# Optimization experiments

Measured on AMD Instinct MI355X. Metric: run time of the kernel, lower is better.

## Reference

```python
import jax, jax.numpy as jnp
import numpy as np


def setup_inputs() -> dict:
    key = jax.random.key(0)
    ks = jax.random.split(key, 7)
    B, S, C, H, W = 4, 8, 256, 64, 64
    A = 256
    return {
        "x": jax.random.normal(ks[0], (B, S, C, H, W), dtype=jnp.float32),
        "wq": jax.random.normal(ks[1], (A, C), dtype=jnp.float32) * (1.0 / np.sqrt(C)),
        "bq": jax.random.normal(ks[2], (A,), dtype=jnp.float32) * 0.01,
        "wk": jax.random.normal(ks[3], (A, C), dtype=jnp.float32) * (1.0 / np.sqrt(C)),
        "bk": jax.random.normal(ks[4], (A,), dtype=jnp.float32) * 0.01,
        "wv": jax.random.normal(ks[5], (A, C), dtype=jnp.float32) * (1.0 / np.sqrt(C)),
        "bv": jax.random.normal(ks[6], (A,), dtype=jnp.float32) * 0.01,
    }


def reference(x, wq, bq, wk, bk, wv, bv):
    B, S, C, H, W = x.shape
    A = wq.shape[0]
    HW = H * W
    scale = 1.0 / (A ** 0.5)

    # 1x1 conv == channel GEMM over flattened spatial dims: [B*S, C, HW] -> [B*S, A, HW]
    xr = x.reshape(B * S, C, HW)
    q = jnp.einsum('ncp,ac->nap', xr, wq) + bq[None, :, None]
    k = jnp.einsum('ncp,ac->nap', xr, wk) + bk[None, :, None]
    v = jnp.einsum('ncp,ac->nap', xr, wv) + bv[None, :, None]

    # [B, S, A, HW]
    q = q.reshape(B, S, A, HW)
    k = k.reshape(B, S, A, HW)
    v = v.reshape(B, S, A, HW)

    # Faithful to torch permute+contiguous().view: raw row-major reinterpretation
    # of the trailing [A, S] block as [S, A] (not a transpose).
    q = jnp.transpose(q, (0, 3, 2, 1)).reshape(B * HW, S, A)
    k = jnp.transpose(k, (0, 3, 1, 2)).reshape(B * HW, A, S)
    v = jnp.transpose(v, (0, 3, 2, 1)).reshape(B * HW, S, A)

    scores = jnp.einsum('nsa,nat->nst', q, k) * scale  # [B*HW, S, S]
    weights = jax.nn.softmax(scores, axis=-1)
    attended = jnp.einsum('nst,nta->nsa', weights, v)  # [B*HW, S, A]

    # view(B, H, W, A, S) raw reshape, then permute(0,4,3,1,2) -> [B, S, A, H, W]
    attended = attended.reshape(B, H, W, A, S)
    attended = jnp.transpose(attended, (0, 4, 3, 1, 2)).reshape(B, S, A, H, W)
    return attended
```

## Files before the change

### kernel.cpp

```cpp
#include <hip/hip_runtime.h>
#include <hip/hip_bf16.h>

typedef __hip_bfloat16 bf16;
typedef __attribute__((ext_vector_type(8))) short short8;
typedef __attribute__((ext_vector_type(4))) float f32x4;

#define MFMA16(A, B, C) __builtin_amdgcn_mfma_f32_16x16x32_bf16((A), (B), (C), 0, 0, 0)

__device__ __forceinline__ void bar_lds() {
    asm volatile("s_waitcnt lgkmcnt(0)\n\ts_barrier" ::: "memory");
}

__device__ __forceinline__ unsigned pkbf(float a, float b) {
    __hip_bfloat162 h2 = __float22bfloat162_rn(make_float2(a, b));
    return *reinterpret_cast<unsigned*>(&h2);
}

__global__ __launch_bounds__(256) void prep_w(const float* __restrict__ wq,
                                              const float* __restrict__ wk,
                                              const float* __restrict__ wv,
                                              bf16* __restrict__ wsW)
{
    const int t = (int)blockIdx.x * 256 + (int)threadIdx.x;
    const int lane = t & 63, kk = (t >> 6) & 7, mt = (t >> 9) & 15, proj = t >> 13;
    const float* W = (proj == 0) ? wq : ((proj == 1) ? wk : wv);
    const int row = mt * 16 + (lane & 15);
    const int col = kk * 32 + (lane >> 4) * 8;
    bf16* dst = wsW + (size_t)t * 8;
#pragma unroll
    for (int j = 0; j < 8; ++j) dst[j] = __float2bfloat16(W[row * 256 + col + j]);
}

#define QLB 8192
#define KLB 41984
#define VLB 8192
#define PLB 75776

__global__ __launch_bounds__(512, 4)
void fused_sa(const float* __restrict__ x,
              const float* __restrict__ bq, const float* __restrict__ bk,
              const float* __restrict__ bv,
              const bf16* __restrict__ wsW,
              float* __restrict__ out)
{
    __shared__ __align__(16) char SM[76928];

    const int tid = (int)threadIdx.x;
    const int l = tid & 63, w = tid >> 6, h = l >> 4, c15 = l & 15;
    const int p = c15 & 7, beta = c15 >> 3;

    const int wg = ((int)blockIdx.x & 7) * 256 + ((int)blockIdx.x >> 3);
    const int b = wg >> 9, p0 = (wg & 511) * 8;

    const short8* wsv = (const short8*)wsW;
    const int p2 = (l & 3) * 2, chi = l >> 2;
    const size_t xbase = ((size_t)((b * 8 + w) * 256)) * 4096 + p0 + p2;

    f32x4 aQ0[4] = {}, aQ1[4] = {}, aK0[4] = {}, aK1[4] = {};
    {
        float2 xr[4];
#pragma unroll
        for (int i = 0; i < 4; ++i)
            xr[i] = *(const float2*)&x[xbase + (size_t)(i * 16 + chi) * 4096];

        for (int cc = 0; cc < 4; ++cc) {
            if (cc) bar_lds();
#pragma unroll
            for (int i = 0; i < 4; ++i) {
                const int c = i * 16 + chi;
                const int r0 = w * 8 + p2, r1 = r0 + 1;
                *(bf16*)(SM + ((r0 * 128 + c * 2) ^ ((r0 & 7) << 4))) = __float2bfloat16(xr[i].x);
                *(bf16*)(SM + ((r1 * 128 + c * 2) ^ ((r1 & 7) << 4))) = __float2bfloat16(xr[i].y);
            }
            if (cc < 3) {
#pragma unroll
                for (int i = 0; i < 4; ++i)
                    xr[i] = *(const float2*)&x[xbase + (size_t)((cc + 1) * 64 + i * 16 + chi) * 4096];
            }
            bar_lds();
#pragma unroll
            for (int k2 = 0; k2 < 2; ++k2) {
                const int kg = cc * 2 + k2;
                const short8 fQ0 = wsv[((0 * 16 + 2 * w)     * 8 + kg) * 64 + l];
                const short8 fQ1 = wsv[((0 * 16 + 2 * w + 1) * 8 + kg) * 64 + l];
                const short8 fK0 = wsv[((1 * 16 + 2 * w)     * 8 + kg) * 64 + l];
                const short8 fK1 = wsv[((1 * 16 + 2 * w + 1) * 8 + kg) * 64 + l];
#pragma unroll
                for (int nt = 0; nt < 4; ++nt) {
                    const int row = nt * 16 + c15;
                    const short8 bx = *(const short8*)(SM +
                        ((row * 128 + (k2 * 32 + h * 8) * 2) ^ ((row & 7) << 4)));
                    aQ0[nt] = MFMA16(fQ0, bx, aQ0[nt]);
                    aQ1[nt] = MFMA16(fQ1, bx, aQ1[nt]);
                    aK0[nt] = MFMA16(fK0, bx, aK0[nt]);
                    aK1[nt] = MFMA16(fK1, bx, aK1[nt]);
                }
            }
        }
    }

    {
        const float4 b0 = *(const float4*)&bq[(2 * w) * 16 + 4 * h];
        const float4 b1 = *(const float4*)&bq[(2 * w + 1) * 16 + 4 * h];
        const float b0v[4] = {b0.x, b0.y, b0.z, b0.w}, b1v[4] = {b1.x, b1.y, b1.z, b1.w};
#pragma unroll
        for (int r = 0; r < 4; ++r) {
            unsigned wds[4];
#pragma unroll
            for (int nt = 0; nt < 4; ++nt) {
                const float a0 = aQ0[nt][r] + b0v[r];
                const float a1 = aQ1[nt][r] + b1v[r];
                const float send = beta ? a0 : a1;
                const float recv = __shfl_xor(send, 8);
                const float own  = beta ? a1 : a0;
                wds[nt] = beta ? pkbf(recv, own) : pkbf(own, recv);
            }
            const int G = 16 * beta + 4 * h + r;
            *(uint4*)(SM + QLB + ((p * 4224 + w * 528 + G * 16) ^ ((p & 7) << 4))) =
                make_uint4(wds[0], wds[1], wds[2], wds[3]);
        }
    }
    {
        const float4 b0 = *(const float4*)&bk[(2 * w) * 16 + 4 * h];
        const float4 b1 = *(const float4*)&bk[(2 * w + 1) * 16 + 4 * h];
        const float b0v[4] = {b0.x, b0.y, b0.z, b0.w}, b1v[4] = {b1.x, b1.y, b1.z, b1.w};
        const bool lower = (h < 2);
#pragma unroll
        for (int r = 0; r < 4; ++r) {
            const int t = 4 * (h & 1) + r;
#pragma unroll
            for (int nt = 0; nt < 4; ++nt) {
                const float a0 = aK0[nt][r] + b0v[r];
                const float a1 = aK1[nt][r] + b1v[r];
                const float r0 = __shfl_xor(a0, 32);
                const float r1 = __shfl_xor(a1, 32);
                const float j0 = lower ? a0 : r0;
                const float j1 = lower ? r0 : a0;
                const float j2 = lower ? a1 : r1;
                const float j3 = lower ? r1 : a1;
                if ((nt & 1) == (h >> 1)) {
                    const int a = ((2 * nt + beta) * 4 + (w >> 1)) * 8 + (w & 1) * 4;
                    *(uint2*)(SM + KLB + ((p * 4224 + t * 528 + a * 2) ^ ((p & 7) << 4))) =
                        make_uint2(pkbf(j0, j1), pkbf(j2, j3));
                }
            }
        }
    }
    bar_lds();

    if (w < 4) {
        const int q = w, pxr = c15 >> 3, st = c15 & 7;
        const int px = 2 * q + pxr;
        f32x4 sacc = {0.f, 0.f, 0.f, 0.f};
#pragma unroll
        for (int kk = 0; kk < 8; ++kk) {
            const int off = (px * 4224 + st * 528 + (kk * 32 + h * 8) * 2) ^ ((px & 7) << 4);
            const short8 qa = *(const short8*)(SM + QLB + off);
            const short8 kb = *(const short8*)(SM + KLB + off);
            sacc = MFMA16(qa, kb, sacc);
        }
        const bool valid = ((h >> 1) == pxr);
        const int pxo = 2 * q + (h >> 1);
        bf16 (*PL)[9][8] = (bf16 (*)[9][8])(SM + PLB);
#pragma unroll
        for (int r = 0; r < 4; ++r) {
            const float S = sacc[r] * 0.0625f;
            float m = S;
            m = fmaxf(m, __shfl_xor(m, 1));
            m = fmaxf(m, __shfl_xor(m, 2));
            m = fmaxf(m, __shfl_xor(m, 4));
            const float e = __expf(S - m);
            float sm = e;
            sm += __shfl_xor(sm, 1);
            sm += __shfl_xor(sm, 2);
            sm += __shfl_xor(sm, 4);
            if (valid) PL[pxo][4 * (h & 1) + r][st] = __float2bfloat16(e / sm);
        }
    }
    bar_lds();

    const int Mv = ((w >> 1) << 2) | (w & 1);
    f32x4 aV0[4] = {}, aV1[4] = {};
    {
        float2 xr[4];
#pragma unroll
        for (int i = 0; i < 4; ++i)
            xr[i] = *(const float2*)&x[xbase + (size_t)(i * 16 + chi) * 4096];

        for (int cc = 0; cc < 4; ++cc) {
            bar_lds();
#pragma unroll
            for (int i = 0; i < 4; ++i) {
                const int c = i * 16 + chi;
                const int r0 = w * 8 + p2, r1 = r0 + 1;
                *(bf16*)(SM + ((r0 * 128 + c * 2) ^ ((r0 & 7) << 4))) = __float2bfloat16(xr[i].x);
                *(bf16*)(SM + ((r1 * 128 + c * 2) ^ ((r1 & 7) << 4))) = __float2bfloat16(xr[i].y);
            }
            if (cc < 3) {
#pragma unroll
                for (int i = 0; i < 4; ++i)
                    xr[i] = *(const float2*)&x[xbase + (size_t)((cc + 1) * 64 + i * 16 + chi) * 4096];
            }
            bar_lds();
#pragma unroll
            for (int k2 = 0; k2 < 2; ++k2) {
                const int kg = cc * 2 + k2;
                const short8 fV0 = wsv[((2 * 16 + Mv)     * 8 + kg) * 64 + l];
                const short8 fV1 = wsv[((2 * 16 + Mv + 2) * 8 + kg) * 64 + l];
#pragma unroll
                for (int nt = 0; nt < 4; ++nt) {
                    const int row = nt * 16 + c15;
                    const short8 bx = *(const short8*)(SM +
                        ((row * 128 + (k2 * 32 + h * 8) * 2) ^ ((row & 7) << 4)));
                    aV0[nt] = MFMA16(fV0, bx, aV0[nt]);
                    aV1[nt] = MFMA16(fV1, bx, aV1[nt]);
                }
            }
        }
    }

    {
        const float4 b0 = *(const float4*)&bv[Mv * 16 + 4 * h];
        const float4 b1 = *(const float4*)&bv[(Mv + 2) * 16 + 4 * h];
        const float b0v[4] = {b0.x, b0.y, b0.z, b0.w}, b1v[4] = {b1.x, b1.y, b1.z, b1.w};
        const int tp2 = 2 * (w >> 1);
#pragma unroll
        for (int r = 0; r < 4; ++r)
#pragma unroll
            for (int nt = 0; nt < 4; ++nt) {
                const unsigned wd = pkbf(aV0[nt][r] + b0v[r], aV1[nt][r] + b1v[r]);
                const int aV = (16 * (w & 1) + 4 * h + r) * 8 + 2 * nt + beta;
                *(unsigned*)(SM + VLB +
                    ((p * 4096 + aV * 16 + tp2 * 2) ^ (((p ^ (aV >> 3)) & 7) << 4))) = wd;
            }
    }
    bar_lds();

    {
        bf16 (*PL)[9][8] = (bf16 (*)[9][8])(SM + PLB);
        const int pxl = c15 & 3, sl = c15 >> 2;
        const short8 zv = {0, 0, 0, 0, 0, 0, 0, 0};
#pragma unroll
        for (int sg = 0; sg < 2; ++sg) {
            short8 pa[2];
#pragma unroll
            for (int q = 0; q < 2; ++q) {
                const short8 t8 = *(const short8*)&PL[q * 4 + pxl][sg * 4 + sl][0];
                pa[q] = (h == pxl) ? t8 : zv;
            }
            const int s = sg * 4 + h;
#pragma unroll
            for (int ci = 0; ci < 2; ++ci) {
                const int a = (2 * w + ci) * 16 + c15;
                const int s2 = a & 7, a2 = (s << 5) | (a >> 3);
#pragma unroll
                for (int q = 0; q < 2; ++q) {
                    const int px = q * 4 + h;
                    const short8 vb = *(const short8*)(SM + VLB +
                        ((px * 4096 + a * 16) ^ (((px ^ (a >> 3)) & 7) << 4)));
                    f32x4 pacc = {0.f, 0.f, 0.f, 0.f};
                    pacc = MFMA16(pa[q], vb, pacc);
                    *(f32x4*)&out[((size_t)((b * 8 + s2) * 256 + a2)) * 4096 + p0 + q * 4] = pacc;
                }
            }
        }
    }
}

extern "C" void kernel_launch(void* const* d_in, const int* in_sizes, int n_in,
                              void* d_out, int out_size, void* d_ws, size_t ws_size,
                              hipStream_t stream) {
    (void)in_sizes; (void)n_in; (void)out_size; (void)ws_size;
    const float* x  = (const float*)d_in[0];
    const float* wq = (const float*)d_in[1];
    const float* bq = (const float*)d_in[2];
    const float* wk = (const float*)d_in[3];
    const float* bk = (const float*)d_in[4];
    const float* wv = (const float*)d_in[5];
    const float* bv = (const float*)d_in[6];
    float* out = (float*)d_out;
    bf16* wsW  = (bf16*)d_ws;

    hipLaunchKernelGGL(prep_w, dim3(96), dim3(256), 0, stream, wq, wk, wv, wsW);
    hipLaunchKernelGGL(fused_sa, dim3(2048), dim3(512), 0, stream,
                       x, bq, bk, bv, wsW, out);
}
```

Before: 172.5 us.

## Process 16 pixels per block in two halves to write 64-byte output runs

Each block now covers 16 spatial positions instead of 8 and runs the Q/K/softmax and V/PV phases twice, once per 8-pixel half. Probabilities for both halves stay in an enlarged LDS buffer, and the first half's PV results are held in registers. Once the second half is done, each output row is written as 64 contiguous bytes rather than 32-byte pieces. The aim is better write coalescing and half as many blocks, at the cost of more registers, more LDS and less parallelism.

```diff
diff --git a/kernel.cpp b/kernel.cpp
--- a/kernel.cpp
+++ b/kernel.cpp
@@ -36,6 +36,91 @@
 #define VLB 8192
 #define PLB 75776
 
+__device__ __forceinline__ void stage_chunk(char* SM, const float2* xr, int w, int p2, int chi) {
+#pragma unroll
+    for (int i = 0; i < 4; ++i) {
+        const int c = i * 16 + chi;
+        const int r0 = w * 8 + p2, r1 = r0 + 1;
+        *(bf16*)(SM + ((r0 * 128 + c * 2) ^ ((r0 & 7) << 4))) = __float2bfloat16(xr[i].x);
+        *(bf16*)(SM + ((r1 * 128 + c * 2) ^ ((r1 & 7) << 4))) = __float2bfloat16(xr[i].y);
+    }
+}
+
+__device__ __forceinline__ void qk_pass(char* SM, const short8* wsv, const float* x,
+                                        size_t xbase, int l, int w, int h, int c15,
+                                        f32x4 (&aQ0)[4], f32x4 (&aQ1)[4],
+                                        f32x4 (&aK0)[4], f32x4 (&aK1)[4])
+{
+    const int p2 = (l & 3) * 2, chi = l >> 2;
+    float2 xr[4];
+#pragma unroll
+    for (int i = 0; i < 4; ++i)
+        xr[i] = *(const float2*)&x[xbase + (size_t)(i * 16 + chi) * 4096];
+    for (int cc = 0; cc < 4; ++cc) {
+        bar_lds();
+        stage_chunk(SM, xr, w, p2, chi);
+        if (cc < 3) {
+#pragma unroll
+            for (int i = 0; i < 4; ++i)
+                xr[i] = *(const float2*)&x[xbase + (size_t)((cc + 1) * 64 + i * 16 + chi) * 4096];
+        }
+        bar_lds();
+#pragma unroll
+        for (int k2 = 0; k2 < 2; ++k2) {
+            const int kg = cc * 2 + k2;
+            const short8 fQ0 = wsv[((0 * 16 + 2 * w)     * 8 + kg) * 64 + l];
+            const short8 fQ1 = wsv[((0 * 16 + 2 * w + 1) * 8 + kg) * 64 + l];
+            const short8 fK0 = wsv[((1 * 16 + 2 * w)     * 8 + kg) * 64 + l];
+            const short8 fK1 = wsv[((1 * 16 + 2 * w + 1) * 8 + kg) * 64 + l];
+#pragma unroll
+            for (int nt = 0; nt < 4; ++nt) {
+                const int row = nt * 16 + c15;
+                const short8 bx = *(const short8*)(SM +
+                    ((row * 128 + (k2 * 32 + h * 8) * 2) ^ ((row & 7) << 4)));
+                aQ0[nt] = MFMA16(fQ0, bx, aQ0[nt]);
+                aQ1[nt] = MFMA16(fQ1, bx, aQ1[nt]);
+                aK0[nt] = MFMA16(fK0, bx, aK0[nt]);
+                aK1[nt] = MFMA16(fK1, bx, aK1[nt]);
+            }
+        }
+    }
+}
+
+__device__ __forceinline__ void v_pass(char* SM, const short8* wsv, const float* x,
+                                       size_t xbase, int l, int w, int h, int c15, int Mv,
+                                       f32x4 (&aV0)[4], f32x4 (&aV1)[4])
+{
+    const int p2 = (l & 3) * 2, chi = l >> 2;
+    float2 xr[4];
+#pragma unroll
+    for (int i = 0; i < 4; ++i)
+        xr[i] = *(const float2*)&x[xbase + (size_t)(i * 16 + chi) * 4096];
+    for (int cc = 0; cc < 4; ++cc) {
+        bar_lds();
+        stage_chunk(SM, xr, w, p2, chi);
+        if (cc < 3) {
+#pragma unroll
+            for (int i = 0; i < 4; ++i)
+                xr[i] = *(const float2*)&x[xbase + (size_t)((cc + 1) * 64 + i * 16 + chi) * 4096];
+        }
+        bar_lds();
+#pragma unroll
+        for (int k2 = 0; k2 < 2; ++k2) {
+            const int kg = cc * 2 + k2;
+            const short8 fV0 = wsv[((2 * 16 + Mv)     * 8 + kg) * 64 + l];
+            const short8 fV1 = wsv[((2 * 16 + Mv + 2) * 8 + kg) * 64 + l];
+#pragma unroll
+            for (int nt = 0; nt < 4; ++nt) {
+                const int row = nt * 16 + c15;
+                const short8 bx = *(const short8*)(SM +
+                    ((row * 128 + (k2 * 32 + h * 8) * 2) ^ ((row & 7) << 4)));
+                aV0[nt] = MFMA16(fV0, bx, aV0[nt]);
+                aV1[nt] = MFMA16(fV1, bx, aV1[nt]);
+            }
+        }
+    }
+}
+
 __global__ __launch_bounds__(512, 4)
 void fused_sa(const float* __restrict__ x,
               const float* __restrict__ bq, const float* __restrict__ bk,
@@ -43,224 +128,185 @@
               const bf16* __restrict__ wsW,
               float* __restrict__ out)
 {
-    __shared__ __align__(16) char SM[76928];
+    __shared__ __align__(16) char SM[78080];
 
     const int tid = (int)threadIdx.x;
     const int l = tid & 63, w = tid >> 6, h = l >> 4, c15 = l & 15;
     const int p = c15 & 7, beta = c15 >> 3;
 
-    const int wg = ((int)blockIdx.x & 7) * 256 + ((int)blockIdx.x >> 3);
-    const int b = wg >> 9, p0 = (wg & 511) * 8;
+    const int wg = ((int)blockIdx.x & 7) * 128 + ((int)blockIdx.x >> 3);
+    const int b = wg >> 8, p0 = (wg & 255) * 16;
 
     const short8* wsv = (const short8*)wsW;
-    const int p2 = (l & 3) * 2, chi = l >> 2;
-    const size_t xbase = ((size_t)((b * 8 + w) * 256)) * 4096 + p0 + p2;
-
-    f32x4 aQ0[4] = {}, aQ1[4] = {}, aK0[4] = {}, aK1[4] = {};
-    {
-        float2 xr[4];
-#pragma unroll
-        for (int i = 0; i < 4; ++i)
-            xr[i] = *(const float2*)&x[xbase + (size_t)(i * 16 + chi) * 4096];
-
-        for (int cc = 0; cc < 4; ++cc) {
-            if (cc) bar_lds();
-#pragma unroll
-            for (int i = 0; i < 4; ++i) {
-                const int c = i * 16 + chi;
-                const int r0 = w * 8 + p2, r1 = r0 + 1;
-                *(bf16*)(SM + ((r0 * 128 + c * 2) ^ ((r0 & 7) << 4))) = __float2bfloat16(xr[i].x);
-                *(bf16*)(SM + ((r1 * 128 + c * 2) ^ ((r1 & 7) << 4))) = __float2bfloat16(xr[i].y);
-            }
-            if (cc < 3) {
-#pragma unroll
-                for (int i = 0; i < 4; ++i)
-                    xr[i] = *(const float2*)&x[xbase + (size_t)((cc + 1) * 64 + i * 16 + chi) * 4096];
+    const size_t xrow = ((size_t)((b * 8 + w) * 256)) * 4096;
+    const int p2g = (l & 3) * 2;
+
+    bf16 (*PL2)[8][9][8] = (bf16 (*)[8][9][8])(SM + PLB);
+
+#pragma unroll
+    for (int half = 0; half < 2; ++half) {
+        f32x4 aQ0[4] = {}, aQ1[4] = {}, aK0[4] = {}, aK1[4] = {};
+        qk_pass(SM, wsv, x, xrow + (size_t)(p0 + half * 8) + p2g, l, w, h, c15,
+                aQ0, aQ1, aK0, aK1);
+
+        {
+            const float4 b0 = *(const float4*)&bq[(2 * w) * 16 + 4 * h];
+            const float4 b1 = *(const float4*)&bq[(2 * w + 1) * 16 + 4 * h];
+            const float b0v[4] = {b0.x, b0.y, b0.z, b0.w}, b1v[4] = {b1.x, b1.y, b1.z, b1.w};
+#pragma unroll
+            for (int r = 0; r < 4; ++r) {
+                unsigned wds[4];
+#pragma unroll
+                for (int nt = 0; nt < 4; ++nt) {
+                    const float a0 = aQ0[nt][r] + b0v[r];
+                    const float a1 = aQ1[nt][r] + b1v[r];
+                    const float send = beta ? a0 : a1;
+                    const float recv = __shfl_xor(send, 8);
+                    const float own  = beta ? a1 : a0;
+                    wds[nt] = beta ? pkbf(recv, own) : pkbf(own, recv);
+                }
+                const int G = 16 * beta + 4 * h + r;
+                *(uint4*)(SM + QLB + ((p * 4224 + w * 528 + G * 16) ^ ((p & 7) << 4))) =
+                    make_uint4(wds[0], wds[1], wds[2], wds[3]);
+            }
+        }
+        {
+            const float4 b0 = *(const float4*)&bk[(2 * w) * 16 + 4 * h];
+            const float4 b1 = *(const float4*)&bk[(2 * w + 1) * 16 + 4 * h];
+            const float b0v[4] = {b0.x, b0.y, b0.z, b0.w}, b1v[4] = {b1.x, b1.y, b1.z, b1.w};
+            const bool lower = (h < 2);
+#pragma unroll
+            for (int r = 0; r < 4; ++r) {
+                const int t = 4 * (h & 1) + r;
+#pragma unroll
+                for (int nt = 0; nt < 4; ++nt) {
+                    const float a0 = aK0[nt][r] + b0v[r];
+                    const float a1 = aK1[nt][r] + b1v[r];
+                    const float r0 = __shfl_xor(a0, 32);
+                    const float r1 = __shfl_xor(a1, 32);
+                    const float j0 = lower ? a0 : r0;
+                    const float j1 = lower ? r0 : a0;
+                    const float j2 = lower ? a1 : r1;
+                    const float j3 = lower ? r1 : a1;
+                    if ((nt & 1) == (h >> 1)) {
+                        const int a = ((2 * nt + beta) * 4 + (w >> 1)) * 8 + (w & 1) * 4;
+                        *(uint2*)(SM + KLB + ((p * 4224 + t * 528 + a * 2) ^ ((p & 7) << 4))) =
+                            make_uint2(pkbf(j0, j1), pkbf(j2, j3));
+                    }
+                }
+            }
+        }
+        bar_lds();
+
+        if (w < 4) {
+            const int q = w, pxr = c15 >> 3, st = c15 & 7;
+            const int px = 2 * q + pxr;
+            f32x4 sacc = {0.f, 0.f, 0.f, 0.f};
+#pragma unroll
+            for (int kk = 0; kk < 8; ++kk) {
+                const int off = (px * 4224 + st * 528 + (kk * 32 + h * 8) * 2) ^ ((px & 7) << 4);
+                const short8 qa = *(const short8*)(SM + QLB + off);
+                const short8 kb = *(const short8*)(SM + KLB + off);
+                sacc = MFMA16(qa, kb, sacc);
+            }
+            const bool valid = ((h >> 1) == pxr);
+            const int pxo = 2 * q + (h >> 1);
+#pragma unroll
+            for (int r = 0; r < 4; ++r) {
+                const float S = sacc[r] * 0.0625f;
+                float m = S;
+                m = fmaxf(m, __shfl_xor(m, 1));
+                m = fmaxf(m, __shfl_xor(m, 2));
+                m = fmaxf(m, __shfl_xor(m, 4));
+                const float e = __expf(S - m);
+                float sm = e;
+                sm += __shfl_xor(sm, 1);
+                sm += __shfl_xor(sm, 2);
+                sm += __shfl_xor(sm, 4);
+                if (valid) PL2[half][pxo][4 * (h & 1) + r][st] = __float2bfloat16(e / sm);
+            }
+        }
+        bar_lds();
+    }
+
+    const int Mv = ((w >> 1) << 2) | (w & 1);
+    const int pxl = c15 & 3, sl = c15 >> 2;
+    const short8 zv = {0, 0, 0, 0, 0, 0, 0, 0};
+    f32x4 oA[2][2][2];
+
+#pragma unroll
+    for (int half = 0; half < 2; ++half) {
+        f32x4 aV0[4] = {}, aV1[4] = {};
+        v_pass(SM, wsv, x, xrow + (size_t)(p0 + half * 8) + p2g, l, w, h, c15, Mv, aV0, aV1);
+
+        {
+            const float4 b0 = *(const float4*)&bv[Mv * 16 + 4 * h];
+            const float4 b1 = *(const float4*)&bv[(Mv + 2) * 16 + 4 * h];
+            const float b0v[4] = {b0.x, b0.y, b0.z, b0.w}, b1v[4] = {b1.x, b1.y, b1.z, b1.w};
+            const int tp2 = 2 * (w >> 1);
+#pragma unroll
+            for (int r = 0; r < 4; ++r)
+#pragma unroll
+                for (int nt = 0; nt < 4; ++nt) {
+                    const unsigned wd = pkbf(aV0[nt][r] + b0v[r], aV1[nt][r] + b1v[r]);
+                    const int aV = (16 * (w & 1) + 4 * h + r) * 8 + 2 * nt + beta;
+                    *(unsigned*)(SM + VLB +
+                        ((p * 4096 + aV * 16 + tp2 * 2) ^ (((p ^ (aV >> 3)) & 7) << 4))) = wd;
+                }
+        }
+        bar_lds();
+
+        if (half == 0) {
+#pragma unroll
+            for (int sg = 0; sg < 2; ++sg) {
+                short8 pa[2];
+#pragma unroll
+                for (int q = 0; q < 2; ++q) {
+                    const short8 t8 = *(const short8*)&PL2[0][q * 4 + pxl][sg * 4 + sl][0];
+                    pa[q] = (h == pxl) ? t8 : zv;
+                }
+#pragma unroll
+                for (int ci = 0; ci < 2; ++ci) {
+                    const int a = (2 * w + ci) * 16 + c15;
+#pragma unroll
+                    for (int q = 0; q < 2; ++q) {
+                        const int px = q * 4 + h;
+                        const short8 vb = *(const short8*)(SM + VLB +
+                            ((px * 4096 + a * 16) ^ (((px ^ (a >> 3)) & 7) << 4)));
+                        f32x4 pacc = {0.f, 0.f, 0.f, 0.f};
+                        oA[sg][ci][q] = MFMA16(pa[q], vb, pacc);
+                    }
+                }
             }
             bar_lds();
-#pragma unroll
-            for (int k2 = 0; k2 < 2; ++k2) {
-                const int kg = cc * 2 + k2;
-                const short8 fQ0 = wsv[((0 * 16 + 2 * w)     * 8 + kg) * 64 + l];
-                const short8 fQ1 = wsv[((0 * 16 + 2 * w + 1) * 8 + kg) * 64 + l];
-                const short8 fK0 = wsv[((1 * 16 + 2 * w)     * 8 + kg) * 64 + l];
-                const short8 fK1 = wsv[((1 * 16 + 2 * w + 1) * 8 + kg) * 64 + l];
-#pragma unroll
-                for (int nt = 0; nt < 4; ++nt) {
-                    const int row = nt * 16 + c15;
-                    const short8 bx = *(const short8*)(SM +
-                        ((row * 128 + (k2 * 32 + h * 8) * 2) ^ ((row & 7) << 4)));
-                    aQ0[nt] = MFMA16(fQ0, bx, aQ0[nt]);
-                    aQ1[nt] = MFMA16(fQ1, bx, aQ1[nt]);
-                    aK0[nt] = MFMA16(fK0, bx, aK0[nt]);
-                    aK1[nt] = MFMA16(fK1, bx, aK1[nt]);
-                }
-            }
-        }
-    }
-
-    {
-        const float4 b0 = *(const float4*)&bq[(2 * w) * 16 + 4 * h];
-        const float4 b1 = *(const float4*)&bq[(2 * w + 1) * 16 + 4 * h];
-        const float b0v[4] = {b0.x, b0.y, b0.z, b0.w}, b1v[4] = {b1.x, b1.y, b1.z, b1.w};
-#pragma unroll
-        for (int r = 0; r < 4; ++r) {
-            unsigned wds[4];
-#pragma unroll
-            for (int nt = 0; nt < 4; ++nt) {
-                const float a0 = aQ0[nt][r] + b0v[r];
-                const float a1 = aQ1[nt][r] + b1v[r];
-                const float send = beta ? a0 : a1;
-                const float recv = __shfl_xor(send, 8);
-                const float own  = beta ? a1 : a0;
-                wds[nt] = beta ? pkbf(recv, own) : pkbf(own, recv);
-            }
-            const int G = 16 * beta + 4 * h + r;
-            *(uint4*)(SM + QLB + ((p * 4224 + w * 528 + G * 16) ^ ((p & 7) << 4))) =
-                make_uint4(wds[0], wds[1], wds[2], wds[3]);
-        }
-    }
-    {
-        const float4 b0 = *(const float4*)&bk[(2 * w) * 16 + 4 * h];
-        const float4 b1 = *(const float4*)&bk[(2 * w + 1) * 16 + 4 * h];
-        const float b0v[4] = {b0.x, b0.y, b0.z, b0.w}, b1v[4] = {b1.x, b1.y, b1.z, b1.w};
-        const bool lower = (h < 2);
-#pragma unroll
-        for (int r = 0; r < 4; ++r) {
-            const int t = 4 * (h & 1) + r;
-#pragma unroll
-            for (int nt = 0; nt < 4; ++nt) {
-                const float a0 = aK0[nt][r] + b0v[r];
-                const float a1 = aK1[nt][r] + b1v[r];
-                const float r0 = __shfl_xor(a0, 32);
-                const float r1 = __shfl_xor(a1, 32);
-                const float j0 = lower ? a0 : r0;
-                const float j1 = lower ? r0 : a0;
-                const float j2 = lower ? a1 : r1;
-                const float j3 = lower ? r1 : a1;
-                if ((nt & 1) == (h >> 1)) {
-                    const int a = ((2 * nt + beta) * 4 + (w >> 1)) * 8 + (w & 1) * 4;
-                    *(uint2*)(SM + KLB + ((p * 4224 + t * 528 + a * 2) ^ ((p & 7) << 4))) =
-                        make_uint2(pkbf(j0, j1), pkbf(j2, j3));
-                }
-            }
-        }
-    }
-    bar_lds();
-
-    if (w < 4) {
-        const int q = w, pxr = c15 >> 3, st = c15 & 7;
-        const int px = 2 * q + pxr;
-        f32x4 sacc = {0.f, 0.f, 0.f, 0.f};
-#pragma unroll
-        for (int kk = 0; kk < 8; ++kk) {
-            const int off = (px * 4224 + st * 528 + (kk * 32 + h * 8) * 2) ^ ((px & 7) << 4);
-            const short8 qa = *(const short8*)(SM + QLB + off);
-            const short8 kb = *(const short8*)(SM + KLB + off);
-            sacc = MFMA16(qa, kb, sacc);
-        }
-        const bool valid = ((h >> 1) == pxr);
-        const int pxo = 2 * q + (h >> 1);
-        bf16 (*PL)[9][8] = (bf16 (*)[9][8])(SM + PLB);
-#pragma unroll
-        for (int r = 0; r < 4; ++r) {
-            const float S = sacc[r] * 0.0625f;
-            float m = S;
-            m = fmaxf(m, __shfl_xor(m, 1));
-            m = fmaxf(m, __shfl_xor(m, 2));
-            m = fmaxf(m, __shfl_xor(m, 4));
-            const float e = __expf(S - m);
-            float sm = e;
-            sm += __shfl_xor(sm, 1);
-            sm += __shfl_xor(sm, 2);
-            sm += __shfl_xor(sm, 4);
-            if (valid) PL[pxo][4 * (h & 1) + r][st] = __float2bfloat16(e / sm);
-        }
-    }
-    bar_lds();
-
-    const int Mv = ((w >> 1) << 2) | (w & 1);
-    f32x4 aV0[4] = {}, aV1[4] = {};
-    {
-        float2 xr[4];
-#pragma unroll
-        for (int i = 0; i < 4; ++i)
-            xr[i] = *(const float2*)&x[xbase + (size_t)(i * 16 + chi) * 4096];
-
-        for (int cc = 0; cc < 4; ++cc) {
-            bar_lds();
-#pragma unroll
-            for (int i = 0; i < 4; ++i) {
-                const int c = i * 16 + chi;
-                const int r0 = w * 8 + p2, r1 = r0 + 1;
-                *(bf16*)(SM + ((r0 * 128 + c * 2) ^ ((r0 & 7) << 4))) = __float2bfloat16(xr[i].x);
-                *(bf16*)(SM + ((r1 * 128 + c * 2) ^ ((r1 & 7) << 4))) = __float2bfloat16(xr[i].y);
-            }
-            if (cc < 3) {
-#pragma unroll
-                for (int i = 0; i < 4; ++i)
-                    xr[i] = *(const float2*)&x[xbase + (size_t)((cc + 1) * 64 + i * 16 + chi) * 4096];
-            }
-            bar_lds();
-#pragma unroll
-            for (int k2 = 0; k2 < 2; ++k2) {
-                const int kg = cc * 2 + k2;
-                const short8 fV0 = wsv[((2 * 16 + Mv)     * 8 + kg) * 64 + l];
-                const short8 fV1 = wsv[((2 * 16 + Mv + 2) * 8 + kg) * 64 + l];
-#pragma unroll
-                for (int nt = 0; nt < 4; ++nt) {
-                    const int row = nt * 16 + c15;
-                    const short8 bx = *(const short8*)(SM +
-                        ((row * 128 + (k2 * 32 + h * 8) * 2) ^ ((row & 7) << 4)));
-                    aV0[nt] = MFMA16(fV0, bx, aV0[nt]);
-                    aV1[nt] = MFMA16(fV1, bx, aV1[nt]);
-                }
-            }
-        }
-    }
-
-    {
-        const float4 b0 = *(const float4*)&bv[Mv * 16 + 4 * h];
-        const float4 b1 = *(const float4*)&bv[(Mv + 2) * 16 + 4 * h];
-        const float b0v[4] = {b0.x, b0.y, b0.z, b0.w}, b1v[4] = {b1.x, b1.y, b1.z, b1.w};
-        const int tp2 = 2 * (w >> 1);
-#pragma unroll
-        for (int r = 0; r < 4; ++r)
-#pragma unroll
-            for (int nt = 0; nt < 4; ++nt) {
-                const unsigned wd = pkbf(aV0[nt][r] + b0v[r], aV1[nt][r] + b1v[r]);
-                const int aV = (16 * (w & 1) + 4 * h + r) * 8 + 2 * nt + beta;
-                *(unsigned*)(SM + VLB +
-                    ((p * 4096 + aV * 16 + tp2 * 2) ^ (((p ^ (aV >> 3)) & 7) << 4))) = wd;
-            }
-    }
-    bar_lds();
-
-    {
-        bf16 (*PL)[9][8] = (bf16 (*)[9][8])(SM + PLB);
-        const int pxl = c15 & 3, sl = c15 >> 2;
-        const short8 zv = {0, 0, 0, 0, 0, 0, 0, 0};
-#pragma unroll
-        for (int sg = 0; sg < 2; ++sg) {
-            short8 pa[2];
-#pragma unroll
-            for (int q = 0; q < 2; ++q) {
-                const short8 t8 = *(const short8*)&PL[q * 4 + pxl][sg * 4 + sl][0];
-                pa[q] = (h == pxl) ? t8 : zv;
-            }
-            const int s = sg * 4 + h;
-#pragma unroll
-            for (int ci = 0; ci < 2; ++ci) {
-                const int a = (2 * w + ci) * 16 + c15;
-                const int s2 = a & 7, a2 = (s << 5) | (a >> 3);
+        } else {
+#pragma unroll
+            for (int sg = 0; sg < 2; ++sg) {
+                short8 pa[2];
 #pragma unroll
                 for (int q = 0; q < 2; ++q) {
-                    const int px = q * 4 + h;
-                    const short8 vb = *(const short8*)(SM + VLB +
-                        ((px * 4096 + a * 16) ^ (((px ^ (a >> 3)) & 7) << 4)));
-                    f32x4 pacc = {0.f, 0.f, 0.f, 0.f};
-                    pacc = MFMA16(pa[q], vb, pacc);
-                    *(f32x4*)&out[((size_t)((b * 8 + s2) * 256 + a2)) * 4096 + p0 + q * 4] = pacc;
+                    const short8 t8 = *(const short8*)&PL2[1][q * 4 + pxl][sg * 4 + sl][0];
+                    pa[q] = (h == pxl) ? t8 : zv;
+                }
+                const int s = sg * 4 + h;
+#pragma unroll
+                for (int ci = 0; ci < 2; ++ci) {
+                    const int a = (2 * w + ci) * 16 + c15;
+                    const int s2 = a & 7, a2 = (s << 5) | (a >> 3);
+                    f32x4 pb[2];
+#pragma unroll
+                    for (int q = 0; q < 2; ++q) {
+                        const int px = q * 4 + h;
+                        const short8 vb = *(const short8*)(SM + VLB +
+                            ((px * 4096 + a * 16) ^ (((px ^ (a >> 3)) & 7) << 4)));
+                        f32x4 pacc = {0.f, 0.f, 0.f, 0.f};
+                        pb[q] = MFMA16(pa[q], vb, pacc);
+                    }
+                    float* op = &out[((size_t)((b * 8 + s2) * 256 + a2)) * 4096 + p0];
+                    *(f32x4*)&op[0]  = oA[sg][ci][0];
+                    *(f32x4*)&op[4]  = oA[sg][ci][1];
+                    *(f32x4*)&op[8]  = pb[0];
+                    *(f32x4*)&op[12] = pb[1];
                 }
             }
         }
@@ -282,6 +328,6 @@
     bf16* wsW  = (bf16*)d_ws;
 
     hipLaunchKernelGGL(prep_w, dim3(96), dim3(256), 0, stream, wq, wk, wv, wsW);
-    hipLaunchKernelGGL(fused_sa, dim3(2048), dim3(512), 0, stream,
+    hipLaunchKernelGGL(fused_sa, dim3(1024), dim3(512), 0, stream,
                        x, bq, bk, bv, wsW, out);
 }
```

Result: slower. 366.4 us (+112.4%).
